# Kernel tuning notes

Measured on AMD Instinct MI355X. Metric: run time of the kernel, lower is better.

## Reference

```python
import jax, jax.numpy as jnp
import numpy as np

DIM = 768
NUM_HEADS = 12
HEAD_DIM = DIM // NUM_HEADS
SCALE = HEAD_DIM ** -0.5


def setup_inputs() -> dict:
    key = jax.random.key(0)
    k_x, k_qkv, k_proj, k_pb = jax.random.split(key, 4)
    B, N = 8, 1024
    x = jax.random.normal(k_x, (B, N, DIM), dtype=jnp.float32)
    # nn.Linear(dim, 3*dim, bias=False): weight [3*dim, dim]
    w_qkv = jax.random.normal(k_qkv, (3 * DIM, DIM), dtype=jnp.float32) * (DIM ** -0.5)
    # nn.Linear(dim, dim): weight [dim, dim], bias [dim]
    w_proj = jax.random.normal(k_proj, (DIM, DIM), dtype=jnp.float32) * (DIM ** -0.5)
    b_proj = jax.random.normal(k_pb, (DIM,), dtype=jnp.float32) * 0.01
    return {"x": x, "w_qkv": w_qkv, "w_proj": w_proj, "b_proj": b_proj}


def reference(x, w_qkv, w_proj, b_proj):
    B, N, C = x.shape
    H, D = NUM_HEADS, HEAD_DIM
    # qkv: [B, N, 3C] -> [3, B, H, N, D]
    qkv = jnp.einsum('bnc,oc->bno', x, w_qkv)
    qkv = qkv.reshape(B, N, 3, H, D).transpose(2, 0, 3, 1, 4)
    q, k, v = qkv[0], qkv[1], qkv[2]
    # scores in float32 (module explicitly casts to float)
    attn = jnp.einsum('bhnd,bhmd->bhnm', q.astype(jnp.float32), k.astype(jnp.float32)) * SCALE
    attn = jax.nn.softmax(attn, axis=-1)
    attn = jnp.where(jnp.isnan(attn), 0.0, attn)  # masked_fill nan -> 0
    out = jnp.einsum('bhnm,bhmd->bhnd', attn, v.astype(jnp.float32))
    out = out.transpose(0, 2, 1, 3).reshape(B, N, C)
    out = jnp.einsum('bnc,oc->bno', out, w_proj) + b_proj
    return out
```

## Files before the change

kernel.cpp:

```cpp
#include <hip/hip_runtime.h>

typedef _Float16 half8 __attribute__((ext_vector_type(8)));
typedef _Float16 half4 __attribute__((ext_vector_type(4)));
typedef float f32x4 __attribute__((ext_vector_type(4)));

#define NHEAD 12
#define HDIM  64
#define SEQ   1024
#define CDIM  768
#define O3    2304
#define MTOK  8192

__device__ __forceinline__ void load_lds16(const void* g, void* l) {
  __builtin_amdgcn_global_load_lds(
      (const __attribute__((address_space(1))) unsigned int*)g,
      (__attribute__((address_space(3))) unsigned int*)l, 16, 0, 0);
}

__global__ __launch_bounds__(256) void cast_f2h(const float* __restrict__ in,
                                                _Float16* __restrict__ out) {
  size_t i = ((size_t)blockIdx.x * 256 + threadIdx.x) * 4;
  float4 v = *reinterpret_cast<const float4*>(in + i);
  half4 h;
  h[0] = (_Float16)v.x; h[1] = (_Float16)v.y; h[2] = (_Float16)v.z; h[3] = (_Float16)v.w;
  *reinterpret_cast<half4*>(out + i) = h;
}


__global__ __launch_bounds__(512) void qkv_gemm(const _Float16* __restrict__ A,
                                                const _Float16* __restrict__ Bw,
                                                _Float16* __restrict__ Qh,
                                                _Float16* __restrict__ Kh,
                                                _Float16* __restrict__ VT) {
  __shared__ _Float16 Ab[3][256 * 64];
  __shared__ _Float16 Bb[3][128 * 64];
  const int tid  = threadIdx.x;
  const int lane = tid & 63;
  const int wv   = tid >> 6;
  const int wm   = wv >> 1;
  const int wn   = wv & 1;
  const int fr   = lane & 15;
  const int kg   = lane >> 4;

  const int lin = blockIdx.x;
  const int xk  = lin & 7;
  const int xj  = lin >> 3;
  const int m0  = (xk * 4 + (xj & 3)) * 256;
  const int n0  = (xj >> 2) * 128;

  f32x4 acc[4][4];
#pragma unroll
  for (int i = 0; i < 4; ++i)
#pragma unroll
    for (int j = 0; j < 4; ++j) acc[i][j] = (f32x4){0.f, 0.f, 0.f, 0.f};

  auto stageT = [&](int bi, int kt) {
#pragma unroll
    for (int r = 0; r < 4; ++r) {
      const int c = r * 512 + tid;
      const int row = c >> 3, cc = c & 7;
      load_lds16(A + (size_t)(m0 + row) * CDIM + kt + ((cc ^ (row & 7)) * 8), &Ab[bi][c * 8]);
    }
#pragma unroll
    for (int r = 0; r < 2; ++r) {
      const int c = r * 512 + tid;
      const int row = c >> 3, cc = c & 7;
      load_lds16(Bw + (size_t)(n0 + row) * CDIM + kt + ((cc ^ (row & 7)) * 8), &Bb[bi][c * 8]);
    }
  };

  auto computeT = [&](int bi) {
#pragma unroll
    for (int kk = 0; kk < 2; ++kk) {
      half8 a[4], b[4];
#pragma unroll
      for (int i = 0; i < 4; ++i) {
        const int row = wm * 64 + i * 16 + fr;
        a[i] = *reinterpret_cast<const half8*>(
            &Ab[bi][row * 64 + (((kk * 4 + kg) ^ (row & 7)) * 8)]);
      }
#pragma unroll
      for (int j = 0; j < 4; ++j) {
        const int row = wn * 64 + j * 16 + fr;
        b[j] = *reinterpret_cast<const half8*>(
            &Bb[bi][row * 64 + (((kk * 4 + kg) ^ (row & 7)) * 8)]);
      }
      __builtin_amdgcn_s_setprio(1);
#pragma unroll
      for (int i = 0; i < 4; ++i)
#pragma unroll
        for (int j = 0; j < 4; ++j)
          acc[i][j] = __builtin_amdgcn_mfma_f32_16x16x32_f16(a[i], b[j], acc[i][j], 0, 0, 0);
      __builtin_amdgcn_s_setprio(0);
    }
  };

  stageT(0, 0);
  stageT(1, 64);
#pragma unroll
  for (int t = 0; t < 12; ++t) {
    if (t + 1 < 12) { asm volatile("s_waitcnt vmcnt(6)" ::: "memory"); }
    else            { asm volatile("s_waitcnt vmcnt(0)" ::: "memory"); }
    __builtin_amdgcn_s_barrier();
    __builtin_amdgcn_sched_barrier(0);
    if (t + 2 < 12) stageT((t + 2) % 3, (t + 2) * 64);
    computeT(t % 3);
    __builtin_amdgcn_sched_barrier(0);
  }

  const float QSCALE = 0.125f * 1.44269504088896f;
  const int t0    = n0 / CDIM;
  const int hbase = n0 - t0 * CDIM;
#pragma unroll
  for (int i = 0; i < 4; ++i) {
    const int mrow = m0 + wm * 64 + i * 16 + kg * 4;
#pragma unroll
    for (int j = 0; j < 4; ++j) {
      const int hd = hbase + wn * 64 + j * 16 + fr;
      const int h  = hd >> 6, d = hd & 63;
#pragma unroll
      for (int r = 0; r < 4; ++r) {
        const int m  = mrow + r;
        const int bb = m >> 10, nn = m & 1023;
        const float v = acc[i][j][r];
        if (t0 == 0)
          Qh[(((size_t)(bb * NHEAD + h)) << 16) + (nn << 6) + d] = (_Float16)(v * QSCALE);
        else if (t0 == 1)
          Kh[(((size_t)(bb * NHEAD + h)) << 16) + (nn << 6) + d] = (_Float16)v;
        else
          VT[(((size_t)(bb * NHEAD + h)) << 16) + (d << 10) + nn] = (_Float16)v;
      }
    }
  }
}

__global__ __launch_bounds__(512) void attn_kernel(const _Float16* __restrict__ Qh,
                                                   const _Float16* __restrict__ Kh,
                                                   const _Float16* __restrict__ VT,
                                                   _Float16* __restrict__ AO) {
  __shared__ _Float16 Ks[3][64 * 64];
  __shared__ _Float16 Vs[3][64 * 64];
  __shared__ _Float16 Ps[8 * 16 * 64];
  const int tid  = threadIdx.x;
  const int lane = tid & 63;
  const int w    = tid >> 6;
  const int fr   = lane & 15;
  const int kg   = lane >> 4;
  const int kh   = kg * 8;
  const int bh   = blockIdx.x;
  const int qt   = blockIdx.y;
  const int q0   = qt * 128 + w * 16;
  const size_t qkbase = (size_t)bh * SEQ * HDIM;
  char* const psw = (char*)&Ps[w * 16 * 64];

  half8 qb[2];
#pragma unroll
  for (int ks = 0; ks < 2; ++ks)
    qb[ks] = *reinterpret_cast<const half8*>(
        &Qh[qkbase + (size_t)(q0 + fr) * HDIM + ks * 32 + kh]);

  f32x4 O[4];
  float mrun = -__builtin_inff();
  float lrun = 0.f;
#pragma unroll
  for (int fd = 0; fd < 4; ++fd) O[fd] = (f32x4){0.f, 0.f, 0.f, 0.f};

  auto stageKV = [&](int bi, int t) {
    const int kt = t * 64;
    const int row = tid >> 3, cc = tid & 7;
    load_lds16(&Kh[qkbase + (size_t)(kt + row) * HDIM + ((cc ^ (row & 7)) * 8)],
               &Ks[bi][tid * 8]);
    load_lds16(&VT[(size_t)bh * HDIM * SEQ + (size_t)row * SEQ + kt + ((cc ^ (row & 7)) * 8)],
               &Vs[bi][tid * 8]);
  };

  auto computeKV = [&](const _Float16* Ksrc, const _Float16* Vsrc) {
    f32x4 st[4];
#pragma unroll
    for (int fc = 0; fc < 4; ++fc) st[fc] = (f32x4){0.f, 0.f, 0.f, 0.f};
#pragma unroll
    for (int ks = 0; ks < 2; ++ks) {
#pragma unroll
      for (int fc = 0; fc < 4; ++fc) {
        const int row = fc * 16 + fr;
        const int colh = ks * 32 + kh;
        half8 ka = *reinterpret_cast<const half8*>(
            &Ksrc[row * 64 + (((colh >> 3) ^ (row & 7)) << 3)]);
        st[fc] = __builtin_amdgcn_mfma_f32_16x16x32_f16(ka, qb[ks], st[fc], 0, 0, 0);
      }
    }

    float mx = st[0][0];
#pragma unroll
    for (int fc = 0; fc < 4; ++fc)
#pragma unroll
      for (int r = 0; r < 4; ++r) mx = fmaxf(mx, st[fc][r]);
    mx = fmaxf(mx, __shfl_xor(mx, 16));
    mx = fmaxf(mx, __shfl_xor(mx, 32));

    if (!__all(mx - mrun <= 8.f)) {
      const float mnew = fmaxf(mrun, mx);
      const float corr = exp2f(mrun - mnew);
      mrun = mnew;
      lrun *= corr;
#pragma unroll
      for (int r = 0; r < 4; ++r) {
        const float c4 = __shfl(corr, kg * 4 + r);
#pragma unroll
        for (int fd = 0; fd < 4; ++fd) O[fd][r] *= c4;
      }
    }

    float rs = 0.f;
#pragma unroll
    for (int fc = 0; fc < 4; ++fc)
#pragma unroll
      for (int r = 0; r < 4; ++r) {
        const float p = exp2f(st[fc][r] - mrun);
        st[fc][r] = p;
        rs += p;
      }
    rs += __shfl_xor(rs, 16);
    rs += __shfl_xor(rs, 32);
    lrun += rs;

#pragma unroll
    for (int fc = 0; fc < 4; ++fc) {
      half4 pk;
      pk[0] = (_Float16)st[fc][0];
      pk[1] = (_Float16)st[fc][1];
      pk[2] = (_Float16)st[fc][2];
      pk[3] = (_Float16)st[fc][3];
      const int slot = (fc * 2 + (kg >> 1)) ^ (fr & 7);
      *reinterpret_cast<half4*>(psw + fr * 128 + slot * 16 + (kg & 1) * 8) = pk;
    }

#pragma unroll
    for (int ks = 0; ks < 2; ++ks) {
      const int rslot = (ks * 4 + kg) ^ (fr & 7);
      half8 pa = *reinterpret_cast<half8*>(psw + fr * 128 + rslot * 16);
#pragma unroll
      for (int fd = 0; fd < 4; ++fd) {
        const int row = fd * 16 + fr;
        const int colh = ks * 32 + kh;
        half8 vb = *reinterpret_cast<const half8*>(
            &Vsrc[row * 64 + (((colh >> 3) ^ (row & 7)) << 3)]);
        O[fd] = __builtin_amdgcn_mfma_f32_16x16x32_f16(pa, vb, O[fd], 0, 0, 0);
      }
    }
  };

  stageKV(0, 0);
  stageKV(1, 1);
#pragma unroll
  for (int t = 0; t < 16; ++t) {
    if (t + 1 < 16) { asm volatile("s_waitcnt vmcnt(2)" ::: "memory"); }
    else            { asm volatile("s_waitcnt vmcnt(0)" ::: "memory"); }
    __builtin_amdgcn_s_barrier();
    __builtin_amdgcn_sched_barrier(0);
    if (t + 2 < 16) stageKV((t + 2) % 3, t + 2);
    computeKV(&Ks[t % 3][0], &Vs[t % 3][0]);
  }

  const int b = bh / NHEAD, h = bh % NHEAD;
  const float linv = 1.0f / lrun;
#pragma unroll
  for (int r = 0; r < 4; ++r) {
    const float lq = __shfl(linv, kg * 4 + r);
    const int n = q0 + kg * 4 + r;
#pragma unroll
    for (int fd = 0; fd < 4; ++fd)
      AO[((size_t)b * SEQ + n) * CDIM + h * HDIM + fd * 16 + fr] =
          (_Float16)(O[fd][r] * lq);
  }
}

__global__ __launch_bounds__(512) void proj_gemm(const _Float16* __restrict__ A,
                                                 const _Float16* __restrict__ Bw,
                                                 const float* __restrict__ bias,
                                                 float* __restrict__ Out) {
  __shared__ _Float16 Ab[3][256 * 64];
  __shared__ _Float16 Bb[3][128 * 64];
  const int tid  = threadIdx.x;
  const int lane = tid & 63;
  const int wv   = tid >> 6;
  const int wm   = wv >> 1;
  const int wn   = wv & 1;
  const int fr   = lane & 15;
  const int kg   = lane >> 4;

  const int lin = blockIdx.x;
  const int xk  = lin & 7;
  const int xj  = lin >> 3;
  const int m0  = (xk * 4 + (xj & 3)) * 256;
  const int n0  = (xj >> 2) * 128;

  f32x4 acc[4][4];
#pragma unroll
  for (int i = 0; i < 4; ++i)
#pragma unroll
    for (int j = 0; j < 4; ++j) acc[i][j] = (f32x4){0.f, 0.f, 0.f, 0.f};

  auto stageT = [&](int bi, int kt) {
#pragma unroll
    for (int r = 0; r < 4; ++r) {
      const int c = r * 512 + tid;
      const int row = c >> 3, cc = c & 7;
      load_lds16(A + (size_t)(m0 + row) * CDIM + kt + ((cc ^ (row & 7)) * 8), &Ab[bi][c * 8]);
    }
#pragma unroll
    for (int r = 0; r < 2; ++r) {
      const int c = r * 512 + tid;
      const int row = c >> 3, cc = c & 7;
      load_lds16(Bw + (size_t)(n0 + row) * CDIM + kt + ((cc ^ (row & 7)) * 8), &Bb[bi][c * 8]);
    }
  };

  auto computeT = [&](int bi) {
#pragma unroll
    for (int kk = 0; kk < 2; ++kk) {
      half8 a[4], b[4];
#pragma unroll
      for (int i = 0; i < 4; ++i) {
        const int row = wm * 64 + i * 16 + fr;
        a[i] = *reinterpret_cast<const half8*>(
            &Ab[bi][row * 64 + (((kk * 4 + kg) ^ (row & 7)) * 8)]);
      }
#pragma unroll
      for (int j = 0; j < 4; ++j) {
        const int row = wn * 64 + j * 16 + fr;
        b[j] = *reinterpret_cast<const half8*>(
            &Bb[bi][row * 64 + (((kk * 4 + kg) ^ (row & 7)) * 8)]);
      }
      __builtin_amdgcn_s_setprio(1);
#pragma unroll
      for (int i = 0; i < 4; ++i)
#pragma unroll
        for (int j = 0; j < 4; ++j)
          acc[i][j] = __builtin_amdgcn_mfma_f32_16x16x32_f16(a[i], b[j], acc[i][j], 0, 0, 0);
      __builtin_amdgcn_s_setprio(0);
    }
  };

  stageT(0, 0);
  stageT(1, 64);
#pragma unroll
  for (int t = 0; t < 12; ++t) {
    if (t + 1 < 12) { asm volatile("s_waitcnt vmcnt(6)" ::: "memory"); }
    else            { asm volatile("s_waitcnt vmcnt(0)" ::: "memory"); }
    __builtin_amdgcn_s_barrier();
    __builtin_amdgcn_sched_barrier(0);
    if (t + 2 < 12) stageT((t + 2) % 3, (t + 2) * 64);
    computeT(t % 3);
    __builtin_amdgcn_sched_barrier(0);
  }

#pragma unroll
  for (int i = 0; i < 4; ++i) {
    const int mrow = m0 + wm * 64 + i * 16 + kg * 4;
#pragma unroll
    for (int j = 0; j < 4; ++j) {
      const int ocol = n0 + wn * 64 + j * 16 + fr;
      const float bv = bias[ocol];
#pragma unroll
      for (int r = 0; r < 4; ++r)
        Out[(size_t)(mrow + r) * CDIM + ocol] = acc[i][j][r] + bv;
    }
  }
}

extern "C" void kernel_launch(void* const* d_in, const int* in_sizes, int n_in,
                              void* d_out, int out_size, void* d_ws, size_t ws_size,
                              hipStream_t stream) {
  const float* x     = (const float*)d_in[0];
  const float* wqkv  = (const float*)d_in[1];
  const float* wproj = (const float*)d_in[2];
  const float* bproj = (const float*)d_in[3];
  float* out = (float*)d_out;

  char* ws = (char*)d_ws;
  _Float16* x_h     = (_Float16*)(ws);
  _Float16* wqkv_h  = (_Float16*)(ws + 12582912);
  _Float16* wproj_h = (_Float16*)(ws + 16121856);
  _Float16* Qh      = (_Float16*)(ws + 17301504);
  _Float16* Kh      = (_Float16*)(ws + 29884416);
  _Float16* VT      = (_Float16*)(ws + 42467328);
  _Float16* AOh     = (_Float16*)(ws + 55050240);

  cast_f2h<<<6291456 / 1024, 256, 0, stream>>>(x, x_h);
  cast_f2h<<<1769472 / 1024, 256, 0, stream>>>(wqkv, wqkv_h);
  cast_f2h<<<589824 / 1024, 256, 0, stream>>>(wproj, wproj_h);

  qkv_gemm<<<576, 512, 0, stream>>>(x_h, wqkv_h, Qh, Kh, VT);
  attn_kernel<<<dim3(96, 8), 512, 0, stream>>>(Qh, Kh, VT, AOh);
  proj_gemm<<<192, 512, 0, stream>>>(AOh, wproj_h, bproj, out);
}
```

Measured before the change: 142.8 us.

## Split GEMM k-tile into two phases interleaving LDS reads, staging and MFMAs

Restructures the QKV and projection GEMM main loops so each 64-wide k-tile runs as two phases. Each phase issues its LDS fragment reads, then half of the next tile's global-to-LDS loads, then a barrier and an lgkmcnt wait, then 16 MFMAs. This spreads the async loads across the compute and keeps waves in step, aiming to overlap memory and LDS traffic with matrix math. It also changes the wave-to-tile mapping (wm = wv&3, wn = wv>>2). The cost is two extra block barriers per k-tile.

```diff
diff --git a/kernel.cpp b/kernel.cpp
--- a/kernel.cpp
+++ b/kernel.cpp
@@ -10,6 +10,9 @@
 #define CDIM  768
 #define O3    2304
 #define MTOK  8192
+
+#define SB  __builtin_amdgcn_sched_barrier(0)
+#define BAR __builtin_amdgcn_s_barrier()
 
 __device__ __forceinline__ void load_lds16(const void* g, void* l) {
   __builtin_amdgcn_global_load_lds(
@@ -37,8 +40,8 @@
   const int tid  = threadIdx.x;
   const int lane = tid & 63;
   const int wv   = tid >> 6;
-  const int wm   = wv >> 1;
-  const int wn   = wv & 1;
+  const int wm   = wv & 3;
+  const int wn   = wv >> 2;
   const int fr   = lane & 15;
   const int kg   = lane >> 4;
 
@@ -54,58 +57,58 @@
 #pragma unroll
     for (int j = 0; j < 4; ++j) acc[i][j] = (f32x4){0.f, 0.f, 0.f, 0.f};
 
-  auto stageT = [&](int bi, int kt) {
-#pragma unroll
-    for (int r = 0; r < 4; ++r) {
-      const int c = r * 512 + tid;
+  auto stagePh = [&](int bi, int kt, int h) {
+#pragma unroll
+    for (int r = 0; r < 2; ++r) {
+      const int c = h * 1024 + r * 512 + tid;
       const int row = c >> 3, cc = c & 7;
       load_lds16(A + (size_t)(m0 + row) * CDIM + kt + ((cc ^ (row & 7)) * 8), &Ab[bi][c * 8]);
     }
-#pragma unroll
-    for (int r = 0; r < 2; ++r) {
-      const int c = r * 512 + tid;
+    {
+      const int c = h * 512 + tid;
       const int row = c >> 3, cc = c & 7;
       load_lds16(Bw + (size_t)(n0 + row) * CDIM + kt + ((cc ^ (row & 7)) * 8), &Bb[bi][c * 8]);
     }
   };
 
-  auto computeT = [&](int bi) {
-#pragma unroll
-    for (int kk = 0; kk < 2; ++kk) {
-      half8 a[4], b[4];
-#pragma unroll
-      for (int i = 0; i < 4; ++i) {
-        const int row = wm * 64 + i * 16 + fr;
-        a[i] = *reinterpret_cast<const half8*>(
-            &Ab[bi][row * 64 + (((kk * 4 + kg) ^ (row & 7)) * 8)]);
-      }
-#pragma unroll
-      for (int j = 0; j < 4; ++j) {
-        const int row = wn * 64 + j * 16 + fr;
-        b[j] = *reinterpret_cast<const half8*>(
-            &Bb[bi][row * 64 + (((kk * 4 + kg) ^ (row & 7)) * 8)]);
-      }
-      __builtin_amdgcn_s_setprio(1);
-#pragma unroll
-      for (int i = 0; i < 4; ++i)
-#pragma unroll
-        for (int j = 0; j < 4; ++j)
-          acc[i][j] = __builtin_amdgcn_mfma_f32_16x16x32_f16(a[i], b[j], acc[i][j], 0, 0, 0);
-      __builtin_amdgcn_s_setprio(0);
-    }
-  };
-
-  stageT(0, 0);
-  stageT(1, 64);
+  auto phase = [&](int bi, int kk, int sbi, int skt, bool doStage) {
+    half8 a[4], b[4];
+#pragma unroll
+    for (int i = 0; i < 4; ++i) {
+      const int row = wm * 64 + i * 16 + fr;
+      a[i] = *reinterpret_cast<const half8*>(
+          &Ab[bi][row * 64 + (((kk * 4 + kg) ^ (row & 7)) * 8)]);
+    }
+#pragma unroll
+    for (int j = 0; j < 4; ++j) {
+      const int row = wn * 64 + j * 16 + fr;
+      b[j] = *reinterpret_cast<const half8*>(
+          &Bb[bi][row * 64 + (((kk * 4 + kg) ^ (row & 7)) * 8)]);
+    }
+    if (doStage) stagePh(sbi, skt, kk);
+    SB;
+    BAR;
+    asm volatile("s_waitcnt lgkmcnt(0)" ::: "memory");
+    SB;
+    __builtin_amdgcn_s_setprio(1);
+#pragma unroll
+    for (int i = 0; i < 4; ++i)
+#pragma unroll
+      for (int j = 0; j < 4; ++j)
+        acc[i][j] = __builtin_amdgcn_mfma_f32_16x16x32_f16(a[i], b[j], acc[i][j], 0, 0, 0);
+    __builtin_amdgcn_s_setprio(0);
+  };
+
+  stagePh(0, 0, 0);  stagePh(0, 0, 1);
+  stagePh(1, 64, 0); stagePh(1, 64, 1);
 #pragma unroll
   for (int t = 0; t < 12; ++t) {
-    if (t + 1 < 12) { asm volatile("s_waitcnt vmcnt(6)" ::: "memory"); }
-    else            { asm volatile("s_waitcnt vmcnt(0)" ::: "memory"); }
-    __builtin_amdgcn_s_barrier();
-    __builtin_amdgcn_sched_barrier(0);
-    if (t + 2 < 12) stageT((t + 2) % 3, (t + 2) * 64);
-    computeT(t % 3);
-    __builtin_amdgcn_sched_barrier(0);
+    if (t < 11) { asm volatile("s_waitcnt vmcnt(6)" ::: "memory"); }
+    else        { asm volatile("s_waitcnt vmcnt(0)" ::: "memory"); }
+    BAR; SB;
+    const bool st = (t + 2 < 12);
+    phase(t % 3, 0, (t + 2) % 3, (t + 2) * 64, st);
+    phase(t % 3, 1, (t + 2) % 3, (t + 2) * 64, st);
   }
 
   const float QSCALE = 0.125f * 1.44269504088896f;
@@ -256,8 +259,7 @@
   for (int t = 0; t < 16; ++t) {
     if (t + 1 < 16) { asm volatile("s_waitcnt vmcnt(2)" ::: "memory"); }
     else            { asm volatile("s_waitcnt vmcnt(0)" ::: "memory"); }
-    __builtin_amdgcn_s_barrier();
-    __builtin_amdgcn_sched_barrier(0);
+    BAR; SB;
     if (t + 2 < 16) stageKV((t + 2) % 3, t + 2);
     computeKV(&Ks[t % 3][0], &Vs[t % 3][0]);
   }
@@ -284,8 +286,8 @@
   const int tid  = threadIdx.x;
   const int lane = tid & 63;
   const int wv   = tid >> 6;
-  const int wm   = wv >> 1;
-  const int wn   = wv & 1;
+  const int wm   = wv & 3;
+  const int wn   = wv >> 2;
   const int fr   = lane & 15;
   const int kg   = lane >> 4;
 
@@ -301,58 +303,58 @@
 #pragma unroll
     for (int j = 0; j < 4; ++j) acc[i][j] = (f32x4){0.f, 0.f, 0.f, 0.f};
 
-  auto stageT = [&](int bi, int kt) {
-#pragma unroll
-    for (int r = 0; r < 4; ++r) {
-      const int c = r * 512 + tid;
+  auto stagePh = [&](int bi, int kt, int h) {
+#pragma unroll
+    for (int r = 0; r < 2; ++r) {
+      const int c = h * 1024 + r * 512 + tid;
       const int row = c >> 3, cc = c & 7;
       load_lds16(A + (size_t)(m0 + row) * CDIM + kt + ((cc ^ (row & 7)) * 8), &Ab[bi][c * 8]);
     }
-#pragma unroll
-    for (int r = 0; r < 2; ++r) {
-      const int c = r * 512 + tid;
+    {
+      const int c = h * 512 + tid;
       const int row = c >> 3, cc = c & 7;
       load_lds16(Bw + (size_t)(n0 + row) * CDIM + kt + ((cc ^ (row & 7)) * 8), &Bb[bi][c * 8]);
     }
   };
 
-  auto computeT = [&](int bi) {
-#pragma unroll
-    for (int kk = 0; kk < 2; ++kk) {
-      half8 a[4], b[4];
-#pragma unroll
-      for (int i = 0; i < 4; ++i) {
-        const int row = wm * 64 + i * 16 + fr;
-        a[i] = *reinterpret_cast<const half8*>(
-            &Ab[bi][row * 64 + (((kk * 4 + kg) ^ (row & 7)) * 8)]);
-      }
-#pragma unroll
-      for (int j = 0; j < 4; ++j) {
-        const int row = wn * 64 + j * 16 + fr;
-        b[j] = *reinterpret_cast<const half8*>(
-            &Bb[bi][row * 64 + (((kk * 4 + kg) ^ (row & 7)) * 8)]);
-      }
-      __builtin_amdgcn_s_setprio(1);
-#pragma unroll
-      for (int i = 0; i < 4; ++i)
-#pragma unroll
-        for (int j = 0; j < 4; ++j)
-          acc[i][j] = __builtin_amdgcn_mfma_f32_16x16x32_f16(a[i], b[j], acc[i][j], 0, 0, 0);
-      __builtin_amdgcn_s_setprio(0);
-    }
-  };
-
-  stageT(0, 0);
-  stageT(1, 64);
+  auto phase = [&](int bi, int kk, int sbi, int skt, bool doStage) {
+    half8 a[4], b[4];
+#pragma unroll
+    for (int i = 0; i < 4; ++i) {
+      const int row = wm * 64 + i * 16 + fr;
+      a[i] = *reinterpret_cast<const half8*>(
+          &Ab[bi][row * 64 + (((kk * 4 + kg) ^ (row & 7)) * 8)]);
+    }
+#pragma unroll
+    for (int j = 0; j < 4; ++j) {
+      const int row = wn * 64 + j * 16 + fr;
+      b[j] = *reinterpret_cast<const half8*>(
+          &Bb[bi][row * 64 + (((kk * 4 + kg) ^ (row & 7)) * 8)]);
+    }
+    if (doStage) stagePh(sbi, skt, kk);
+    SB;
+    BAR;
+    asm volatile("s_waitcnt lgkmcnt(0)" ::: "memory");
+    SB;
+    __builtin_amdgcn_s_setprio(1);
+#pragma unroll
+    for (int i = 0; i < 4; ++i)
+#pragma unroll
+      for (int j = 0; j < 4; ++j)
+        acc[i][j] = __builtin_amdgcn_mfma_f32_16x16x32_f16(a[i], b[j], acc[i][j], 0, 0, 0);
+    __builtin_amdgcn_s_setprio(0);
+  };
+
+  stagePh(0, 0, 0);  stagePh(0, 0, 1);
+  stagePh(1, 64, 0); stagePh(1, 64, 1);
 #pragma unroll
   for (int t = 0; t < 12; ++t) {
-    if (t + 1 < 12) { asm volatile("s_waitcnt vmcnt(6)" ::: "memory"); }
-    else            { asm volatile("s_waitcnt vmcnt(0)" ::: "memory"); }
-    __builtin_amdgcn_s_barrier();
-    __builtin_amdgcn_sched_barrier(0);
-    if (t + 2 < 12) stageT((t + 2) % 3, (t + 2) * 64);
-    computeT(t % 3);
-    __builtin_amdgcn_sched_barrier(0);
+    if (t < 11) { asm volatile("s_waitcnt vmcnt(6)" ::: "memory"); }
+    else        { asm volatile("s_waitcnt vmcnt(0)" ::: "memory"); }
+    BAR; SB;
+    const bool st = (t + 2 < 12);
+    phase(t % 3, 0, (t + 2) % 3, (t + 2) * 64, st);
+    phase(t % 3, 1, (t + 2) % 3, (t + 2) * 64, st);
   }
 
 #pragma unroll
```

Measured after the change: 144.1 us. About the same (+0.9%).

## Load GEMM fragments directly from global memory into registers, drop LDS staging

Applied to the files above, without the earlier changes.

The QKV and projection GEMMs drop the LDS triple-buffered staging. Each wave now loads its MFMA fragments straight from global memory into registers, double-buffered across k-steps. Tiles shrink to 128x128 with 256 threads, which doubles the grid size. This removes LDS traffic and barriers, but loses cross-wave reuse of the A/B tiles, so it leans on L1/L2 to absorb the duplicate global reads, and those reads are less coalesced.

```diff
diff --git a/kernel.cpp b/kernel.cpp
--- a/kernel.cpp
+++ b/kernel.cpp
@@ -10,6 +10,9 @@
 #define CDIM  768
 #define O3    2304
 #define MTOK  8192
+
+#define SB  __builtin_amdgcn_sched_barrier(0)
+#define BAR __builtin_amdgcn_s_barrier()
 
 __device__ __forceinline__ void load_lds16(const void* g, void* l) {
   __builtin_amdgcn_global_load_lds(
@@ -27,13 +30,11 @@
 }
 
 
-__global__ __launch_bounds__(512) void qkv_gemm(const _Float16* __restrict__ A,
+__global__ __launch_bounds__(256) void qkv_gemm(const _Float16* __restrict__ A,
                                                 const _Float16* __restrict__ Bw,
                                                 _Float16* __restrict__ Qh,
                                                 _Float16* __restrict__ Kh,
                                                 _Float16* __restrict__ VT) {
-  __shared__ _Float16 Ab[3][256 * 64];
-  __shared__ _Float16 Bb[3][128 * 64];
   const int tid  = threadIdx.x;
   const int lane = tid & 63;
   const int wv   = tid >> 6;
@@ -45,8 +46,17 @@
   const int lin = blockIdx.x;
   const int xk  = lin & 7;
   const int xj  = lin >> 3;
-  const int m0  = (xk * 4 + (xj & 3)) * 256;
-  const int n0  = (xj >> 2) * 128;
+  const int n0  = (xj >> 3) * 128;
+  const int m0  = (xk * 8 + (xj & 7)) * 128;
+
+  const _Float16* ap[4];
+  const _Float16* bp[4];
+#pragma unroll
+  for (int i = 0; i < 4; ++i)
+    ap[i] = A + (size_t)(m0 + wm * 64 + i * 16 + fr) * CDIM + kg * 8;
+#pragma unroll
+  for (int j = 0; j < 4; ++j)
+    bp[j] = Bw + (size_t)(n0 + wn * 64 + j * 16 + fr) * CDIM + kg * 8;
 
   f32x4 acc[4][4];
 #pragma unroll
@@ -54,58 +64,33 @@
 #pragma unroll
     for (int j = 0; j < 4; ++j) acc[i][j] = (f32x4){0.f, 0.f, 0.f, 0.f};
 
-  auto stageT = [&](int bi, int kt) {
-#pragma unroll
-    for (int r = 0; r < 4; ++r) {
-      const int c = r * 512 + tid;
-      const int row = c >> 3, cc = c & 7;
-      load_lds16(A + (size_t)(m0 + row) * CDIM + kt + ((cc ^ (row & 7)) * 8), &Ab[bi][c * 8]);
-    }
-#pragma unroll
-    for (int r = 0; r < 2; ++r) {
-      const int c = r * 512 + tid;
-      const int row = c >> 3, cc = c & 7;
-      load_lds16(Bw + (size_t)(n0 + row) * CDIM + kt + ((cc ^ (row & 7)) * 8), &Bb[bi][c * 8]);
-    }
-  };
-
-  auto computeT = [&](int bi) {
-#pragma unroll
-    for (int kk = 0; kk < 2; ++kk) {
-      half8 a[4], b[4];
-#pragma unroll
-      for (int i = 0; i < 4; ++i) {
-        const int row = wm * 64 + i * 16 + fr;
-        a[i] = *reinterpret_cast<const half8*>(
-            &Ab[bi][row * 64 + (((kk * 4 + kg) ^ (row & 7)) * 8)]);
-      }
-#pragma unroll
-      for (int j = 0; j < 4; ++j) {
-        const int row = wn * 64 + j * 16 + fr;
-        b[j] = *reinterpret_cast<const half8*>(
-            &Bb[bi][row * 64 + (((kk * 4 + kg) ^ (row & 7)) * 8)]);
-      }
-      __builtin_amdgcn_s_setprio(1);
-#pragma unroll
-      for (int i = 0; i < 4; ++i)
-#pragma unroll
-        for (int j = 0; j < 4; ++j)
-          acc[i][j] = __builtin_amdgcn_mfma_f32_16x16x32_f16(a[i], b[j], acc[i][j], 0, 0, 0);
-      __builtin_amdgcn_s_setprio(0);
-    }
-  };
-
-  stageT(0, 0);
-  stageT(1, 64);
-#pragma unroll
-  for (int t = 0; t < 12; ++t) {
-    if (t + 1 < 12) { asm volatile("s_waitcnt vmcnt(6)" ::: "memory"); }
-    else            { asm volatile("s_waitcnt vmcnt(0)" ::: "memory"); }
-    __builtin_amdgcn_s_barrier();
-    __builtin_amdgcn_sched_barrier(0);
-    if (t + 2 < 12) stageT((t + 2) % 3, (t + 2) * 64);
-    computeT(t % 3);
-    __builtin_amdgcn_sched_barrier(0);
+  half8 aX[4], bX[4], aY[4], bY[4];
+
+#define LDQ(av, bv, s)                                                        \
+  {                                                                           \
+    _Pragma("unroll") for (int i = 0; i < 4; ++i)                             \
+        av[i] = *reinterpret_cast<const half8*>(ap[i] + (s) * 32);            \
+    _Pragma("unroll") for (int j = 0; j < 4; ++j)                             \
+        bv[j] = *reinterpret_cast<const half8*>(bp[j] + (s) * 32);            \
+  }
+#define MMQ(av, bv)                                                           \
+  {                                                                           \
+    __builtin_amdgcn_s_setprio(1);                                            \
+    _Pragma("unroll") for (int i = 0; i < 4; ++i)                             \
+        _Pragma("unroll") for (int j = 0; j < 4; ++j)                         \
+            acc[i][j] = __builtin_amdgcn_mfma_f32_16x16x32_f16(av[i], bv[j],  \
+                                                               acc[i][j], 0, 0, 0); \
+    __builtin_amdgcn_s_setprio(0);                                            \
+  }
+
+  LDQ(aX, bX, 0);
+  LDQ(aY, bY, 1);
+#pragma unroll
+  for (int s = 0; s < 24; s += 2) {
+    MMQ(aX, bX);
+    if (s + 2 < 24) LDQ(aX, bX, s + 2);
+    MMQ(aY, bY);
+    if (s + 3 < 24) LDQ(aY, bY, s + 3);
   }
 
   const float QSCALE = 0.125f * 1.44269504088896f;
@@ -256,8 +241,7 @@
   for (int t = 0; t < 16; ++t) {
     if (t + 1 < 16) { asm volatile("s_waitcnt vmcnt(2)" ::: "memory"); }
     else            { asm volatile("s_waitcnt vmcnt(0)" ::: "memory"); }
-    __builtin_amdgcn_s_barrier();
-    __builtin_amdgcn_sched_barrier(0);
+    BAR; SB;
     if (t + 2 < 16) stageKV((t + 2) % 3, t + 2);
     computeKV(&Ks[t % 3][0], &Vs[t % 3][0]);
   }
@@ -275,12 +259,10 @@
   }
 }
 
-__global__ __launch_bounds__(512) void proj_gemm(const _Float16* __restrict__ A,
+__global__ __launch_bounds__(256) void proj_gemm(const _Float16* __restrict__ A,
                                                  const _Float16* __restrict__ Bw,
                                                  const float* __restrict__ bias,
                                                  float* __restrict__ Out) {
-  __shared__ _Float16 Ab[3][256 * 64];
-  __shared__ _Float16 Bb[3][128 * 64];
   const int tid  = threadIdx.x;
   const int lane = tid & 63;
   const int wv   = tid >> 6;
@@ -292,8 +274,17 @@
   const int lin = blockIdx.x;
   const int xk  = lin & 7;
   const int xj  = lin >> 3;
-  const int m0  = (xk * 4 + (xj & 3)) * 256;
-  const int n0  = (xj >> 2) * 128;
+  const int n0  = (xj >> 3) * 128;
+  const int m0  = (xk * 8 + (xj & 7)) * 128;
+
+  const _Float16* ap[4];
+  const _Float16* bp[4];
+#pragma unroll
+  for (int i = 0; i < 4; ++i)
+    ap[i] = A + (size_t)(m0 + wm * 64 + i * 16 + fr) * CDIM + kg * 8;
+#pragma unroll
+  for (int j = 0; j < 4; ++j)
+    bp[j] = Bw + (size_t)(n0 + wn * 64 + j * 16 + fr) * CDIM + kg * 8;
 
   f32x4 acc[4][4];
 #pragma unroll
@@ -301,58 +292,16 @@
 #pragma unroll
     for (int j = 0; j < 4; ++j) acc[i][j] = (f32x4){0.f, 0.f, 0.f, 0.f};
 
-  auto stageT = [&](int bi, int kt) {
-#pragma unroll
-    for (int r = 0; r < 4; ++r) {
-      const int c = r * 512 + tid;
-      const int row = c >> 3, cc = c & 7;
-      load_lds16(A + (size_t)(m0 + row) * CDIM + kt + ((cc ^ (row & 7)) * 8), &Ab[bi][c * 8]);
-    }
-#pragma unroll
-    for (int r = 0; r < 2; ++r) {
-      const int c = r * 512 + tid;
-      const int row = c >> 3, cc = c & 7;
-      load_lds16(Bw + (size_t)(n0 + row) * CDIM + kt + ((cc ^ (row & 7)) * 8), &Bb[bi][c * 8]);
-    }
-  };
-
-  auto computeT = [&](int bi) {
-#pragma unroll
-    for (int kk = 0; kk < 2; ++kk) {
-      half8 a[4], b[4];
-#pragma unroll
-      for (int i = 0; i < 4; ++i) {
-        const int row = wm * 64 + i * 16 + fr;
-        a[i] = *reinterpret_cast<const half8*>(
-            &Ab[bi][row * 64 + (((kk * 4 + kg) ^ (row & 7)) * 8)]);
-      }
-#pragma unroll
-      for (int j = 0; j < 4; ++j) {
-        const int row = wn * 64 + j * 16 + fr;
-        b[j] = *reinterpret_cast<const half8*>(
-            &Bb[bi][row * 64 + (((kk * 4 + kg) ^ (row & 7)) * 8)]);
-      }
-      __builtin_amdgcn_s_setprio(1);
-#pragma unroll
-      for (int i = 0; i < 4; ++i)
-#pragma unroll
-        for (int j = 0; j < 4; ++j)
-          acc[i][j] = __builtin_amdgcn_mfma_f32_16x16x32_f16(a[i], b[j], acc[i][j], 0, 0, 0);
-      __builtin_amdgcn_s_setprio(0);
-    }
-  };
-
-  stageT(0, 0);
-  stageT(1, 64);
-#pragma unroll
-  for (int t = 0; t < 12; ++t) {
-    if (t + 1 < 12) { asm volatile("s_waitcnt vmcnt(6)" ::: "memory"); }
-    else            { asm volatile("s_waitcnt vmcnt(0)" ::: "memory"); }
-    __builtin_amdgcn_s_barrier();
-    __builtin_amdgcn_sched_barrier(0);
-    if (t + 2 < 12) stageT((t + 2) % 3, (t + 2) * 64);
-    computeT(t % 3);
-    __builtin_amdgcn_sched_barrier(0);
+  half8 aX[4], bX[4], aY[4], bY[4];
+
+  LDQ(aX, bX, 0);
+  LDQ(aY, bY, 1);
+#pragma unroll
+  for (int s = 0; s < 24; s += 2) {
+    MMQ(aX, bX);
+    if (s + 2 < 24) LDQ(aX, bX, s + 2);
+    MMQ(aY, bY);
+    if (s + 3 < 24) LDQ(aY, bY, s + 3);
   }
 
 #pragma unroll
@@ -391,7 +340,7 @@
   cast_f2h<<<1769472 / 1024, 256, 0, stream>>>(wqkv, wqkv_h);
   cast_f2h<<<589824 / 1024, 256, 0, stream>>>(wproj, wproj_h);
 
-  qkv_gemm<<<576, 512, 0, stream>>>(x_h, wqkv_h, Qh, Kh, VT);
+  qkv_gemm<<<1152, 256, 0, stream>>>(x_h, wqkv_h, Qh, Kh, VT);
   attn_kernel<<<dim3(96, 8), 512, 0, stream>>>(Qh, Kh, VT, AOh);
-  proj_gemm<<<192, 512, 0, stream>>>(AOh, wproj_h, bproj, out);
-}
+  proj_gemm<<<384, 256, 0, stream>>>(AOh, wproj_h, bproj, out);
+}
```

Result: slower. 233.5 us (+63.4%).
